# Optimization experiments

Measured on AMD Instinct MI355X. Metric: run time of the kernel, lower is better.

## Reference

```python
import jax, jax.numpy as jnp
import numpy as np

N_SENT, N_DOC, G = 100000, 10000, 32

def _seg_mean_right(x, src, dst, n_dst):
    # DGL GraphConv(norm='right'): sum incoming messages / in_degree (clamped to 1)
    m = jax.ops.segment_sum(x[src], dst, num_segments=n_dst)
    deg = jax.ops.segment_sum(jnp.ones_like(dst, dtype=x.dtype), dst, num_segments=n_dst)
    return m / jnp.maximum(deg, 1.0)[:, None]

def _rel_layer(xs, xd, coeff, basis, loop_w, bias,
               src_ss, dst_ss, src_sd, dst_sd, src_ds, dst_ds):
    # WeightBasis: per-relation weight = sum_b coeff[r,b] * basis[b]
    W = jnp.einsum('rb,bio->rio', coeff, basis)  # [3, in, out]
    # rel 0: sent->doc, rel 1: doc->sent, rel 2: sent->sent; HeteroGraphConv sums per dst ntype
    h_doc = _seg_mean_right(xs, src_sd, dst_sd, N_DOC) @ W[0]
    h_sent = (_seg_mean_right(xd, src_ds, dst_ds, N_SENT) @ W[1]
              + _seg_mean_right(xs, src_ss, dst_ss, N_SENT) @ W[2])
    h_sent = jax.nn.relu(h_sent + xs @ loop_w + bias)
    h_doc = jax.nn.relu(h_doc + xd @ loop_w + bias)
    return h_sent, h_doc

def setup_inputs() -> dict:
    key = jax.random.key(0)
    ks = jax.random.split(key, 20)
    d_in, d_h, d_o = 768, 256, 128
    inp = {
        'x_sent': jax.random.normal(ks[0], (N_SENT, d_in), jnp.float32),
        'x_doc': jax.random.normal(ks[1], (N_DOC, d_in), jnp.float32),
        'coeff1': jax.random.normal(ks[2], (3, 2), jnp.float32),
        'basis1': jax.random.normal(ks[3], (2, d_in, d_h), jnp.float32) * 0.02,
        'loop_w1': jax.random.normal(ks[4], (d_in, d_h), jnp.float32) * 0.02,
        'bias1': jnp.zeros((d_h,), jnp.float32),
        'coeff2': jax.random.normal(ks[5], (3, 2), jnp.float32),
        'basis2': jax.random.normal(ks[6], (2, d_h, d_o), jnp.float32) * 0.05,
        'loop_w2': jax.random.normal(ks[7], (d_h, d_o), jnp.float32) * 0.05,
        'bias2': jnp.zeros((d_o,), jnp.float32),
        'w_score': jax.random.normal(ks[8], (d_o, 1), jnp.float32) * 0.05,
        'b_score': jnp.zeros((1,), jnp.float32),
        'src_ss': jax.random.randint(ks[9], (400000,), 0, N_SENT, jnp.int32),
        'dst_ss': jax.random.randint(ks[10], (400000,), 0, N_SENT, jnp.int32),
        'src_sd': jax.random.randint(ks[11], (100000,), 0, N_SENT, jnp.int32),
        'dst_sd': jax.random.randint(ks[12], (100000,), 0, N_DOC, jnp.int32),
        'src_ds': jax.random.randint(ks[13], (100000,), 0, N_DOC, jnp.int32),
        'dst_ds': jax.random.randint(ks[14], (100000,), 0, N_SENT, jnp.int32),
        'gid_sent': jnp.sort(jax.random.randint(ks[15], (N_SENT,), 0, G, jnp.int32)),
        'gid_doc': jnp.sort(jax.random.randint(ks[16], (N_DOC,), 0, G, jnp.int32)),
        'num_graphs': G,
    }
    return inp

def reference(x_sent, x_doc, coeff1, basis1, loop_w1, bias1,
              coeff2, basis2, loop_w2, bias2, w_score, b_score,
              src_ss, dst_ss, src_sd, dst_sd, src_ds, dst_ds,
              gid_sent, gid_doc, num_graphs):
    h_s, h_d = _rel_layer(x_sent, x_doc, coeff1, basis1, loop_w1, bias1,
                          src_ss, dst_ss, src_sd, dst_sd, src_ds, dst_ds)
    h_s, h_d = _rel_layer(h_s, h_d, coeff2, basis2, loop_w2, bias2,
                          src_ss, dst_ss, src_sd, dst_sd, src_ds, dst_ds)
    # dgl.sum_nodes over batched graph, summed across ntypes
    readout = (jax.ops.segment_sum(h_s, gid_sent, num_segments=num_graphs)
               + jax.ops.segment_sum(h_d, gid_doc, num_segments=num_graphs))
    return readout @ w_score + b_score  # [G, 1]
```

## Files before the change

kernel.cpp:

```cpp
#include <hip/hip_runtime.h>

#define CDIV(a,b) (((a)+(b)-1)/(b))

typedef __attribute__((ext_vector_type(8))) short bf16x8;
typedef __attribute__((ext_vector_type(4))) float floatx4;

__device__ __forceinline__ ushort f2bf(float x) {
    unsigned u = __float_as_uint(x);
    return (ushort)((u + 0x7fffu + ((u >> 16) & 1u)) >> 16);
}
__device__ __forceinline__ float bflo(unsigned v) { return __uint_as_float(v << 16); }
__device__ __forceinline__ float bfhi(unsigned v) { return __uint_as_float(v & 0xffff0000u); }

__device__ __forceinline__ void load_lds16(const ushort* g, ushort* l) {
    __builtin_amdgcn_global_load_lds(
        (const __attribute__((address_space(1))) void*)g,
        (__attribute__((address_space(3))) void*)l, 16, 0, 0);
}



__global__ void zero_f4(float4* __restrict__ p, long long n4) {
    long long i = blockIdx.x * 256LL + threadIdx.x;
    if (i < n4) p[i] = make_float4(0.f, 0.f, 0.f, 0.f);
}

__global__ void fill_w5(ushort* __restrict__ BsT, ushort* __restrict__ BdT,
                        const float* __restrict__ basis, const float* __restrict__ loopw,
                        const float* __restrict__ coeff, int K, int N, long long KN) {
    long long i = blockIdx.x * 256LL + threadIdx.x;
    if (i >= KN) return;
    int k = (int)(i % K), n = (int)(i / K);
    int sec = blockIdx.y;
    float val;
    if (sec == 2 || sec == 4) {
        val = loopw[(size_t)k * N + n];
    } else {
        int r = (sec == 0) ? 0 : (sec == 1) ? 2 : 1;
        val = coeff[2 * r] * basis[(size_t)k * N + n] + coeff[2 * r + 1] * basis[KN + (size_t)k * N + n];
    }
    ushort* dst = (sec < 3) ? BsT : BdT;
    int col0 = (sec == 0) ? 0 : (sec == 1) ? N : (sec == 2) ? 2 * N : (sec == 3) ? 0 : N;
    int nn = col0 + n;
    dst[(size_t)nn * K + (k & ~63) + ((k & 63) ^ ((nn & 7) << 3))] = f2bf(val);
}


__global__ void accum_deg_all(const int* __restrict__ dss, const int* __restrict__ dds,
                              const int* __restrict__ dsd, int nss, int nds, int nsd,
                              int NS, int* __restrict__ deg) {
    int i = blockIdx.x * 256 + threadIdx.x;
    if (i < nss) atomicAdd(&deg[dss[i]], 1);
    else if (i < nss + nds) atomicAdd(&deg[NS + dds[i - nss]], 1);
    else if (i < nss + nds + nsd) atomicAdd(&deg[2 * NS + dsd[i - nss - nds]], 1);
}

__global__ void scan_p1(const int* __restrict__ deg, int n, int* __restrict__ bsum) {
    __shared__ int sd[256];
    int blk = blockIdx.x, tid = threadIdx.x;
    int i0 = blk * 1024 + tid * 4;
    int s = 0;
#pragma unroll
    for (int j = 0; j < 4; ++j) if (i0 + j < n) s += deg[i0 + j];
    sd[tid] = s; __syncthreads();
    for (int o = 128; o; o >>= 1) {
        if (tid < o) sd[tid] += sd[tid + o];
        __syncthreads();
    }
    if (tid == 0) bsum[blk] = sd[0];
}

__global__ void scan_p2(int* __restrict__ bsum, int nb, int* __restrict__ rowptr, int ntot, int etot) {
    __shared__ int sd[256];
    int tid = threadIdx.x;
    int v = (tid < nb) ? bsum[tid] : 0;
    sd[tid] = v; __syncthreads();
    for (int o = 1; o < 256; o <<= 1) {
        int t = (tid >= o) ? sd[tid - o] : 0;
        __syncthreads();
        sd[tid] += t;
        __syncthreads();
    }
    if (tid < nb) bsum[tid] = sd[tid] - v;
    if (tid == 0) rowptr[ntot] = etot;
}

__global__ void scan_p3(const int* __restrict__ deg, int n, const int* __restrict__ bsum,
                        int* __restrict__ rowptr) {
    __shared__ int sd[256];
    int blk = blockIdx.x, tid = threadIdx.x;
    int i0 = blk * 1024 + tid * 4;
    int v[4]; int s = 0;
#pragma unroll
    for (int j = 0; j < 4; ++j) { v[j] = (i0 + j < n) ? deg[i0 + j] : 0; s += v[j]; }
    sd[tid] = s; __syncthreads();
    for (int o = 1; o < 256; o <<= 1) {
        int t = (tid >= o) ? sd[tid - o] : 0;
        __syncthreads();
        sd[tid] += t;
        __syncthreads();
    }
    int excl = bsum[blk] + sd[tid] - s;
#pragma unroll
    for (int j = 0; j < 4; ++j) {
        if (i0 + j < n) rowptr[i0 + j] = excl;
        excl += v[j];
    }
}

__global__ void fill_csr_all(const int* __restrict__ sss, const int* __restrict__ dss,
                             const int* __restrict__ sds, const int* __restrict__ dds,
                             const int* __restrict__ ssd, const int* __restrict__ dsd,
                             int nss, int nds, int nsd, int NS,
                             const int* __restrict__ rowptr, int* __restrict__ fill,
                             int* __restrict__ col) {
    int i = blockIdx.x * 256 + threadIdx.x;
    int d, s;
    if (i < nss) { d = dss[i]; s = sss[i]; }
    else if (i < nss + nds) { int j = i - nss; d = NS + dds[j]; s = sds[j]; }
    else if (i < nss + nds + nsd) { int j = i - nss - nds; d = 2 * NS + dsd[j]; s = ssd[j]; }
    else return;
    int p = rowptr[d] + atomicAdd(&fill[d], 1);
    col[p] = s;
}

template<bool AF32>
__global__ __launch_bounds__(256) void gemm_any(
    const void* __restrict__ Araw, const ushort* __restrict__ Bt, ushort* __restrict__ C,
    int M, int K, int N, int BNX) {
    const int nwg = gridDim.x;
    const int orig = blockIdx.x;
    const int q = nwg >> 3, r = nwg & 7;
    const int xcd = orig & 7, idx = orig >> 3;
    const int wg = (xcd < r ? xcd * (q + 1) : r * (q + 1) + (xcd - r) * q) + idx;
    const int bn = (wg % BNX) * 128;
    const long long bm = (long long)(wg / BNX) * 128LL;

    __shared__ ushort As[128 * 64];
    __shared__ ushort Bs[128 * 64];
    const int tid = threadIdx.x;
    const int lane = tid & 63, wave = tid >> 6;
    const int mo = (wave & 1) * 64, no = (wave >> 1) * 64;
    const int l15 = lane & 15, quad = lane >> 4;
    const int srow = wave * 8 + (lane >> 3);
    const int bch = (lane & 7) * 8;
    floatx4 acc[4][4] = {};

    for (int k0 = 0; k0 < K; k0 += 64) {
#pragma unroll
        for (int t = 0; t < 4; ++t) {
            int row = t * 32 + srow;
            load_lds16(Bt + (size_t)(bn + row) * K + k0 + bch,
                       Bs + (t * 32 + wave * 8) * 64);
        }
        if (AF32) {
            float4 pre[4][2];
#pragma unroll
            for (int j = 0; j < 4; ++j) {
                int s = j * 256 + tid;
                int arow = s >> 3, ach = s & 7;
                long long ar = bm + arow; if (ar >= M) ar = M - 1;
                const float* ap = (const float*)Araw + ar * (size_t)K + k0 + ach * 8;
                pre[j][0] = *(const float4*)ap;
                pre[j][1] = *(const float4*)(ap + 4);
            }
#pragma unroll
            for (int j = 0; j < 4; ++j) {
                int s = j * 256 + tid;
                int arow = s >> 3, ach = s & 7;
                uint4 o;
                o.x = (unsigned)f2bf(pre[j][0].x) | ((unsigned)f2bf(pre[j][0].y) << 16);
                o.y = (unsigned)f2bf(pre[j][0].z) | ((unsigned)f2bf(pre[j][0].w) << 16);
                o.z = (unsigned)f2bf(pre[j][1].x) | ((unsigned)f2bf(pre[j][1].y) << 16);
                o.w = (unsigned)f2bf(pre[j][1].z) | ((unsigned)f2bf(pre[j][1].w) << 16);
                *(uint4*)(As + arow * 64 + ((ach * 8) ^ ((arow & 7) << 3))) = o;
            }
        } else {
#pragma unroll
            for (int t = 0; t < 4; ++t) {
                int row = t * 32 + srow;
                long long ar = bm + row; if (ar >= M) ar = M - 1;
                load_lds16((const ushort*)Araw + ar * (size_t)K + k0 + bch,
                           As + (t * 32 + wave * 8) * 64);
            }
        }
        __syncthreads();
        bf16x8 af[2][4], bfr[2][4];
#pragma unroll
        for (int h = 0; h < 2; ++h) {
#pragma unroll
            for (int mt = 0; mt < 4; ++mt) {
                int row = mo + mt * 16 + l15;
                af[h][mt] = *(const bf16x8*)(As + row * 64 + ((h * 32 + quad * 8) ^ ((row & 7) << 3)));
            }
#pragma unroll
            for (int nt = 0; nt < 4; ++nt) {
                int row = no + nt * 16 + l15;
                bfr[h][nt] = *(const bf16x8*)(Bs + row * 64 + ((h * 32 + quad * 8) ^ ((row & 7) << 3)));
            }
        }
#pragma unroll
        for (int h = 0; h < 2; ++h)
#pragma unroll
            for (int mt = 0; mt < 4; ++mt)
#pragma unroll
                for (int nt = 0; nt < 4; ++nt)
                    acc[mt][nt] = __builtin_amdgcn_mfma_f32_16x16x32_bf16(af[h][mt], bfr[h][nt], acc[mt][nt], 0, 0, 0);
        __syncthreads();
    }
#pragma unroll
    for (int mt = 0; mt < 4; ++mt)
#pragma unroll
        for (int i = 0; i < 4; ++i) {
            long long row = bm + mo + mt * 16 + quad * 4 + i;
            if (row < M) {
#pragma unroll
                for (int nt = 0; nt < 4; ++nt)
                    C[row * (size_t)N + bn + no + nt * 16 + l15] = f2bf(acc[mt][nt][i]);
            }
        }
}


__global__ __launch_bounds__(256) void gather_l1(
    const ushort* __restrict__ ys, const ushort* __restrict__ yd,
    const int* __restrict__ rowptr, const int* __restrict__ col,
    const float* __restrict__ bias, ushort* __restrict__ h1s, ushort* __restrict__ h1d,
    int NS, int ND) {
    int d = blockIdx.x * 4 + (threadIdx.x >> 6);
    int lane = threadIdx.x & 63;
    int cb = lane * 4;
    float b0 = bias[cb], b1 = bias[cb + 1], b2 = bias[cb + 2], b3 = bias[cb + 3];
    if (d < NS) {
        float a0 = 0, a1 = 0, a2 = 0, a3 = 0;
        int s0 = rowptr[d], s1 = rowptr[d + 1];
        int e = s0;
        for (; e + 4 <= s1; e += 4) {
            int sA = col[e], sB = col[e + 1], sC = col[e + 2], sD = col[e + 3];
            uint2 vA = *(const uint2*)(ys + (size_t)sA * 768 + 256 + cb);
            uint2 vB = *(const uint2*)(ys + (size_t)sB * 768 + 256 + cb);
            uint2 vC = *(const uint2*)(ys + (size_t)sC * 768 + 256 + cb);
            uint2 vD = *(const uint2*)(ys + (size_t)sD * 768 + 256 + cb);
            a0 += bflo(vA.x) + bflo(vB.x) + bflo(vC.x) + bflo(vD.x);
            a1 += bfhi(vA.x) + bfhi(vB.x) + bfhi(vC.x) + bfhi(vD.x);
            a2 += bflo(vA.y) + bflo(vB.y) + bflo(vC.y) + bflo(vD.y);
            a3 += bfhi(vA.y) + bfhi(vB.y) + bfhi(vC.y) + bfhi(vD.y);
        }
        for (; e < s1; ++e) {
            int s = col[e];
            uint2 v = *(const uint2*)(ys + (size_t)s * 768 + 256 + cb);
            a0 += bflo(v.x); a1 += bfhi(v.x); a2 += bflo(v.y); a3 += bfhi(v.y);
        }
        float inv = 1.f / (float)max(s1 - s0, 1);
        float m0 = a0 * inv, m1 = a1 * inv, m2 = a2 * inv, m3 = a3 * inv;
        a0 = a1 = a2 = a3 = 0.f;
        int t0 = rowptr[NS + d], t1 = rowptr[NS + d + 1];
        for (e = t0; e < t1; ++e) {
            int s = col[e];
            uint2 v = *(const uint2*)(yd + (size_t)s * 512 + cb);
            a0 += bflo(v.x); a1 += bfhi(v.x); a2 += bflo(v.y); a3 += bfhi(v.y);
        }
        inv = 1.f / (float)max(t1 - t0, 1);
        uint2 lv = *(const uint2*)(ys + (size_t)d * 768 + 512 + cb);
        float h0 = fmaxf(m0 + a0 * inv + bflo(lv.x) + b0, 0.f);
        float h1 = fmaxf(m1 + a1 * inv + bfhi(lv.x) + b1, 0.f);
        float h2 = fmaxf(m2 + a2 * inv + bflo(lv.y) + b2, 0.f);
        float h3 = fmaxf(m3 + a3 * inv + bfhi(lv.y) + b3, 0.f);
        uint2 o;
        o.x = (unsigned)f2bf(h0) | ((unsigned)f2bf(h1) << 16);
        o.y = (unsigned)f2bf(h2) | ((unsigned)f2bf(h3) << 16);
        int pos = (cb & ~63) + ((cb & 63) ^ ((d & 7) << 3));
        *(uint2*)(h1s + (size_t)d * 256 + pos) = o;
    } else if (d < NS + ND) {
        int dd = d - NS;
        float a0 = 0, a1 = 0, a2 = 0, a3 = 0;
        int s0 = rowptr[2 * NS + dd], s1 = rowptr[2 * NS + dd + 1];
        int e = s0;
        for (; e + 4 <= s1; e += 4) {
            int sA = col[e], sB = col[e + 1], sC = col[e + 2], sD = col[e + 3];
            uint2 vA = *(const uint2*)(ys + (size_t)sA * 768 + cb);
            uint2 vB = *(const uint2*)(ys + (size_t)sB * 768 + cb);
            uint2 vC = *(const uint2*)(ys + (size_t)sC * 768 + cb);
            uint2 vD = *(const uint2*)(ys + (size_t)sD * 768 + cb);
            a0 += bflo(vA.x) + bflo(vB.x) + bflo(vC.x) + bflo(vD.x);
            a1 += bfhi(vA.x) + bfhi(vB.x) + bfhi(vC.x) + bfhi(vD.x);
            a2 += bflo(vA.y) + bflo(vB.y) + bflo(vC.y) + bflo(vD.y);
            a3 += bfhi(vA.y) + bfhi(vB.y) + bfhi(vC.y) + bfhi(vD.y);
        }
        for (; e < s1; ++e) {
            int s = col[e];
            uint2 v = *(const uint2*)(ys + (size_t)s * 768 + cb);
            a0 += bflo(v.x); a1 += bfhi(v.x); a2 += bflo(v.y); a3 += bfhi(v.y);
        }
        float inv = 1.f / (float)max(s1 - s0, 1);
        uint2 lv = *(const uint2*)(yd + (size_t)dd * 512 + 256 + cb);
        float h0 = fmaxf(a0 * inv + bflo(lv.x) + b0, 0.f);
        float h1 = fmaxf(a1 * inv + bfhi(lv.x) + b1, 0.f);
        float h2 = fmaxf(a2 * inv + bflo(lv.y) + b2, 0.f);
        float h3 = fmaxf(a3 * inv + bfhi(lv.y) + b3, 0.f);
        uint2 o;
        o.x = (unsigned)f2bf(h0) | ((unsigned)f2bf(h1) << 16);
        o.y = (unsigned)f2bf(h2) | ((unsigned)f2bf(h3) << 16);
        int pos = (cb & ~63) + ((cb & 63) ^ ((dd & 7) << 3));
        *(uint2*)(h1d + (size_t)dd * 256 + pos) = o;
    }
}

__global__ __launch_bounds__(256) void gather_l2(
    const ushort* __restrict__ ys, const ushort* __restrict__ yd,
    const int* __restrict__ rowptr, const int* __restrict__ col,
    const float* __restrict__ bias, const float* __restrict__ w,
    const int* __restrict__ gid_s, const int* __restrict__ gid_d,
    float* __restrict__ out, int NS, int ND, int G) {
    __shared__ float part[4][32];
    const int tid = threadIdx.x;
    const int lane = tid & 63, wv = tid >> 6;
    const int cb = lane * 2;
    const float w0 = w[cb], w1 = w[cb + 1];
    const float b0 = bias[cb], b1 = bias[cb + 1];
    float racc = 0.f;
    const int nw = gridDim.x * 4;
    for (int d = blockIdx.x * 4 + wv; d < NS + ND; d += nw) {
        float h0, h1; int g;
        if (d < NS) {
            float a0 = 0.f, a1 = 0.f;
            int s0 = rowptr[d], s1 = rowptr[d + 1];
            int e = s0;
            for (; e + 4 <= s1; e += 4) {
                int sA = col[e], sB = col[e + 1], sC = col[e + 2], sD = col[e + 3];
                unsigned vA = *(const unsigned*)(ys + (size_t)sA * 384 + 128 + cb);
                unsigned vB = *(const unsigned*)(ys + (size_t)sB * 384 + 128 + cb);
                unsigned vC = *(const unsigned*)(ys + (size_t)sC * 384 + 128 + cb);
                unsigned vD = *(const unsigned*)(ys + (size_t)sD * 384 + 128 + cb);
                a0 += bflo(vA) + bflo(vB) + bflo(vC) + bflo(vD);
                a1 += bfhi(vA) + bfhi(vB) + bfhi(vC) + bfhi(vD);
            }
            for (; e < s1; ++e) {
                int s = col[e];
                unsigned v = *(const unsigned*)(ys + (size_t)s * 384 + 128 + cb);
                a0 += bflo(v); a1 += bfhi(v);
            }
            float inv = 1.f / (float)max(s1 - s0, 1);
            float m0 = a0 * inv, m1 = a1 * inv;
            a0 = 0.f; a1 = 0.f;
            int t0 = rowptr[NS + d], t1 = rowptr[NS + d + 1];
            for (e = t0; e < t1; ++e) {
                int s = col[e];
                unsigned v = *(const unsigned*)(yd + (size_t)s * 256 + cb);
                a0 += bflo(v); a1 += bfhi(v);
            }
            inv = 1.f / (float)max(t1 - t0, 1);
            unsigned lv = *(const unsigned*)(ys + (size_t)d * 384 + 256 + cb);
            h0 = fmaxf(m0 + a0 * inv + bflo(lv) + b0, 0.f);
            h1 = fmaxf(m1 + a1 * inv + bfhi(lv) + b1, 0.f);
            g = gid_s[d];
        } else {
            int dd = d - NS;
            float a0 = 0.f, a1 = 0.f;
            int s0 = rowptr[2 * NS + dd], s1 = rowptr[2 * NS + dd + 1];
            int e = s0;
            for (; e + 4 <= s1; e += 4) {
                int sA = col[e], sB = col[e + 1], sC = col[e + 2], sD = col[e + 3];
                unsigned vA = *(const unsigned*)(ys + (size_t)sA * 384 + cb);
                unsigned vB = *(const unsigned*)(ys + (size_t)sB * 384 + cb);
                unsigned vC = *(const unsigned*)(ys + (size_t)sC * 384 + cb);
                unsigned vD = *(const unsigned*)(ys + (size_t)sD * 384 + cb);
                a0 += bflo(vA) + bflo(vB) + bflo(vC) + bflo(vD);
                a1 += bfhi(vA) + bfhi(vB) + bfhi(vC) + bfhi(vD);
            }
            for (; e < s1; ++e) {
                int s = col[e];
                unsigned v = *(const unsigned*)(ys + (size_t)s * 384 + cb);
                a0 += bflo(v); a1 += bfhi(v);
            }
            float inv = 1.f / (float)max(s1 - s0, 1);
            unsigned lv = *(const unsigned*)(yd + (size_t)dd * 256 + 128 + cb);
            h0 = fmaxf(a0 * inv + bflo(lv) + b0, 0.f);
            h1 = fmaxf(a1 * inv + bfhi(lv) + b1, 0.f);
            g = gid_d[dd];
        }
        float sc = h0 * w0 + h1 * w1;
#pragma unroll
        for (int o = 32; o; o >>= 1) sc += __shfl_down(sc, o);
        sc = __shfl(sc, 0);
        if (lane == g) racc += sc;
    }
    if (lane < 32) part[wv][lane] = racc;
    __syncthreads();
    if (tid < G) atomicAdd(&out[tid], part[0][tid] + part[1][tid] + part[2][tid] + part[3][tid]);
}

__global__ void init_out(float* __restrict__ out, const float* __restrict__ b, int G) {
    int i = threadIdx.x;
    if (i < G) out[i] = b[0];
}


extern "C" void kernel_launch(void* const* d_in, const int* in_sizes, int n_in,
                              void* d_out, int out_size, void* d_ws, size_t ws_size,
                              hipStream_t stream) {
    const float* x_sent = (const float*)d_in[0];
    const float* x_doc  = (const float*)d_in[1];
    const float* coeff1 = (const float*)d_in[2];
    const float* basis1 = (const float*)d_in[3];
    const float* loopw1 = (const float*)d_in[4];
    const float* bias1  = (const float*)d_in[5];
    const float* coeff2 = (const float*)d_in[6];
    const float* basis2 = (const float*)d_in[7];
    const float* loopw2 = (const float*)d_in[8];
    const float* bias2  = (const float*)d_in[9];
    const float* wscore = (const float*)d_in[10];
    const float* bscore = (const float*)d_in[11];
    const int* src_ss = (const int*)d_in[12];
    const int* dst_ss = (const int*)d_in[13];
    const int* src_sd = (const int*)d_in[14];
    const int* dst_sd = (const int*)d_in[15];
    const int* src_ds = (const int*)d_in[16];
    const int* dst_ds = (const int*)d_in[17];
    const int* gid_sent = (const int*)d_in[18];
    const int* gid_doc  = (const int*)d_in[19];

    const int DIN = 768, DH = 256, DOo = 128;
    const int NS = in_sizes[0] / DIN;
    const int ND = in_sizes[1] / DIN;
    const int E_SS = in_sizes[12], E_SD = in_sizes[14], E_DS = in_sizes[16];
    const int NTOT = NS + NS + ND;
    const int ETOT = E_SS + E_DS + E_SD;
    const int G = out_size;
    float* out = (float*)d_out;

    char* base = (char*)d_ws;
    size_t off = 0;
    auto alloc = [&](size_t bytes) -> char* {
        char* p = base + off;
        off = (off + bytes + 255) & ~(size_t)255;
        return p;
    };
    ushort* B1sT = (ushort*)alloc((size_t)768 * 768 * 2);
    ushort* B1dT = (ushort*)alloc((size_t)512 * 768 * 2);
    ushort* B2sT = (ushort*)alloc((size_t)384 * 256 * 2);
    ushort* B2dT = (ushort*)alloc((size_t)256 * 256 * 2);
    ushort* ys1 = (ushort*)alloc((size_t)NS * 768 * 2);
    ushort* yd1 = (ushort*)alloc((size_t)ND * 512 * 2);
    ushort* h1s = (ushort*)alloc((size_t)NS * 256 * 2);
    ushort* h1d = (ushort*)alloc((size_t)ND * 256 * 2);
    ushort* ys2 = (ushort*)alloc((size_t)NS * 384 * 2);
    ushort* yd2 = (ushort*)alloc((size_t)ND * 256 * 2);
    int* deg  = (int*)alloc((size_t)2 * NTOT * 4);
    int* fill = deg + NTOT;
    int* rowptr = (int*)alloc((size_t)(NTOT + 1) * 4);
    int* bsum = (int*)alloc(256 * 4);
    int* colall = (int*)alloc((size_t)ETOT * 4);

    long long t1 = (long long)768 * DH, t2 = (long long)256 * DOo;
    fill_w5<<<dim3((unsigned)CDIV(t1, 256), 5), 256, 0, stream>>>(B1sT, B1dT, basis1, loopw1, coeff1, 768, DH, t1);
    fill_w5<<<dim3((unsigned)CDIV(t2, 256), 5), 256, 0, stream>>>(B2sT, B2dT, basis2, loopw2, coeff2, 256, DOo, t2);

    zero_f4<<<(int)CDIV(2 * NTOT / 4, 256), 256, 0, stream>>>((float4*)deg, 2 * NTOT / 4);
    accum_deg_all<<<CDIV(ETOT, 256), 256, 0, stream>>>(dst_ss, dst_ds, dst_sd, E_SS, E_DS, E_SD, NS, deg);
    int nb = CDIV(NTOT, 1024);
    scan_p1<<<nb, 256, 0, stream>>>(deg, NTOT, bsum);
    scan_p2<<<1, 256, 0, stream>>>(bsum, nb, rowptr, NTOT, ETOT);
    scan_p3<<<nb, 256, 0, stream>>>(deg, NTOT, bsum, rowptr);
    fill_csr_all<<<CDIV(ETOT, 256), 256, 0, stream>>>(src_ss, dst_ss, src_ds, dst_ds, src_sd, dst_sd,
                                                      E_SS, E_DS, E_SD, NS, rowptr, fill, colall);

    {
        int mb = CDIV(NS, 128), mb0 = mb / 2;
        int M0 = mb0 * 128;
        gemm_any<true><<<6 * mb0, 256, 0, stream>>>(x_sent, B1sT, ys1, M0, 768, 768, 6);
        gemm_any<true><<<6 * (mb - mb0), 256, 0, stream>>>(
            x_sent + (size_t)M0 * 768, B1sT, ys1 + (size_t)M0 * 768, NS - M0, 768, 768, 6);
    }
    gemm_any<true><<<4 * CDIV(ND, 128), 256, 0, stream>>>(x_doc, B1dT, yd1, ND, 768, 512, 4);

    gather_l1<<<CDIV(NS + ND, 4), 256, 0, stream>>>(ys1, yd1, rowptr, colall, bias1, h1s, h1d, NS, ND);

    gemm_any<false><<<3 * CDIV(NS, 128), 256, 0, stream>>>(h1s, B2sT, ys2, NS, 256, 384, 3);
    gemm_any<false><<<2 * CDIV(ND, 128), 256, 0, stream>>>(h1d, B2dT, yd2, ND, 256, 256, 2);

    init_out<<<1, 64, 0, stream>>>(out, bscore, G);
    gather_l2<<<1100, 256, 0, stream>>>(ys2, yd2, rowptr, colall, bias2, wscore,
                                        gid_sent, gid_doc, out, NS, ND, G);
}
```

Before: 982.0 us.

## Load GEMM A fragments directly from global and double-buffer B in LDS

The GEMM no longer stages the A tile through LDS. Each wave loads its A fragments straight from global memory, converting fp32 to bf16 in registers where needed, while B is double-buffered in LDS so the next tile's loads overlap compute and one barrier per iteration is dropped. The gather_l1 kernel now writes h1 unswizzled, since the layer-2 GEMM reads A rows directly instead of through the swizzled LDS layout. The trade-off is that A loads become strided 16–32 byte per-lane global reads with no LDS reuse across waves, so each A row is fetched by two waves, and loads sit right before the MFMAs, which adds latency exposure.

```diff
diff --git a/kernel.cpp b/kernel.cpp
--- a/kernel.cpp
+++ b/kernel.cpp
@@ -136,8 +136,7 @@
     const int bn = (wg % BNX) * 128;
     const long long bm = (long long)(wg / BNX) * 128LL;
 
-    __shared__ ushort As[128 * 64];
-    __shared__ ushort Bs[128 * 64];
+    __shared__ ushort Bs[2][128 * 64];
     const int tid = threadIdx.x;
     const int lane = tid & 63, wave = tid >> 6;
     const int mo = (wave & 1) * 64, no = (wave >> 1) * 64;
@@ -146,67 +145,60 @@
     const int bch = (lane & 7) * 8;
     floatx4 acc[4][4] = {};
 
-    for (int k0 = 0; k0 < K; k0 += 64) {
+    size_t aoff[4];
+#pragma unroll
+    for (int mt = 0; mt < 4; ++mt) {
+        long long ar = bm + mo + mt * 16 + l15;
+        if (ar >= M) ar = M - 1;
+        aoff[mt] = (size_t)ar * K;
+    }
+
+    auto stageB = [&](int k0, int buf) {
 #pragma unroll
         for (int t = 0; t < 4; ++t) {
             int row = t * 32 + srow;
             load_lds16(Bt + (size_t)(bn + row) * K + k0 + bch,
-                       Bs + (t * 32 + wave * 8) * 64);
-        }
-        if (AF32) {
-            float4 pre[4][2];
-#pragma unroll
-            for (int j = 0; j < 4; ++j) {
-                int s = j * 256 + tid;
-                int arow = s >> 3, ach = s & 7;
-                long long ar = bm + arow; if (ar >= M) ar = M - 1;
-                const float* ap = (const float*)Araw + ar * (size_t)K + k0 + ach * 8;
-                pre[j][0] = *(const float4*)ap;
-                pre[j][1] = *(const float4*)(ap + 4);
-            }
-#pragma unroll
-            for (int j = 0; j < 4; ++j) {
-                int s = j * 256 + tid;
-                int arow = s >> 3, ach = s & 7;
-                uint4 o;
-                o.x = (unsigned)f2bf(pre[j][0].x) | ((unsigned)f2bf(pre[j][0].y) << 16);
-                o.y = (unsigned)f2bf(pre[j][0].z) | ((unsigned)f2bf(pre[j][0].w) << 16);
-                o.z = (unsigned)f2bf(pre[j][1].x) | ((unsigned)f2bf(pre[j][1].y) << 16);
-                o.w = (unsigned)f2bf(pre[j][1].z) | ((unsigned)f2bf(pre[j][1].w) << 16);
-                *(uint4*)(As + arow * 64 + ((ach * 8) ^ ((arow & 7) << 3))) = o;
-            }
-        } else {
-#pragma unroll
-            for (int t = 0; t < 4; ++t) {
-                int row = t * 32 + srow;
-                long long ar = bm + row; if (ar >= M) ar = M - 1;
-                load_lds16((const ushort*)Araw + ar * (size_t)K + k0 + bch,
-                           As + (t * 32 + wave * 8) * 64);
-            }
-        }
-        __syncthreads();
-        bf16x8 af[2][4], bfr[2][4];
-#pragma unroll
-        for (int h = 0; h < 2; ++h) {
-#pragma unroll
-            for (int mt = 0; mt < 4; ++mt) {
-                int row = mo + mt * 16 + l15;
-                af[h][mt] = *(const bf16x8*)(As + row * 64 + ((h * 32 + quad * 8) ^ ((row & 7) << 3)));
-            }
+                       Bs[buf] + (t * 32 + wave * 8) * 64);
+        }
+    };
+
+    stageB(0, 0);
+    int cur = 0;
+    for (int k0 = 0; k0 < K; k0 += 64) {
+        __syncthreads();
+        if (k0 + 64 < K) stageB(k0 + 64, cur ^ 1);
+        bf16x8 bfr[2][4];
+#pragma unroll
+        for (int h = 0; h < 2; ++h)
 #pragma unroll
             for (int nt = 0; nt < 4; ++nt) {
                 int row = no + nt * 16 + l15;
-                bfr[h][nt] = *(const bf16x8*)(Bs + row * 64 + ((h * 32 + quad * 8) ^ ((row & 7) << 3)));
-            }
-        }
-#pragma unroll
-        for (int h = 0; h < 2; ++h)
-#pragma unroll
-            for (int mt = 0; mt < 4; ++mt)
+                bfr[h][nt] = *(const bf16x8*)(Bs[cur] + row * 64 + ((h * 32 + quad * 8) ^ ((row & 7) << 3)));
+            }
+#pragma unroll
+        for (int h = 0; h < 2; ++h) {
+#pragma unroll
+            for (int mt = 0; mt < 4; ++mt) {
+                bf16x8 af;
+                if (AF32) {
+                    const float* ap = (const float*)Araw + aoff[mt] + k0 + h * 32 + quad * 8;
+                    float4 p0 = *(const float4*)ap;
+                    float4 p1 = *(const float4*)(ap + 4);
+                    unsigned w0 = (unsigned)f2bf(p0.x) | ((unsigned)f2bf(p0.y) << 16);
+                    unsigned w1 = (unsigned)f2bf(p0.z) | ((unsigned)f2bf(p0.w) << 16);
+                    unsigned w2 = (unsigned)f2bf(p1.x) | ((unsigned)f2bf(p1.y) << 16);
+                    unsigned w3 = (unsigned)f2bf(p1.z) | ((unsigned)f2bf(p1.w) << 16);
+                    uint4 packed = make_uint4(w0, w1, w2, w3);
+                    af = *(const bf16x8*)&packed;
+                } else {
+                    af = *(const bf16x8*)((const ushort*)Araw + aoff[mt] + k0 + h * 32 + quad * 8);
+                }
 #pragma unroll
                 for (int nt = 0; nt < 4; ++nt)
-                    acc[mt][nt] = __builtin_amdgcn_mfma_f32_16x16x32_bf16(af[h][mt], bfr[h][nt], acc[mt][nt], 0, 0, 0);
-        __syncthreads();
+                    acc[mt][nt] = __builtin_amdgcn_mfma_f32_16x16x32_bf16(af, bfr[h][nt], acc[mt][nt], 0, 0, 0);
+            }
+        }
+        cur ^= 1;
     }
 #pragma unroll
     for (int mt = 0; mt < 4; ++mt)
@@ -269,8 +261,7 @@
         uint2 o;
         o.x = (unsigned)f2bf(h0) | ((unsigned)f2bf(h1) << 16);
         o.y = (unsigned)f2bf(h2) | ((unsigned)f2bf(h3) << 16);
-        int pos = (cb & ~63) + ((cb & 63) ^ ((d & 7) << 3));
-        *(uint2*)(h1s + (size_t)d * 256 + pos) = o;
+        *(uint2*)(h1s + (size_t)d * 256 + cb) = o;
     } else if (d < NS + ND) {
         int dd = d - NS;
         float a0 = 0, a1 = 0, a2 = 0, a3 = 0;
@@ -301,8 +292,7 @@
         uint2 o;
         o.x = (unsigned)f2bf(h0) | ((unsigned)f2bf(h1) << 16);
         o.y = (unsigned)f2bf(h2) | ((unsigned)f2bf(h3) << 16);
-        int pos = (cb & ~63) + ((cb & 63) ^ ((dd & 7) << 3));
-        *(uint2*)(h1d + (size_t)dd * 256 + pos) = o;
+        *(uint2*)(h1d + (size_t)dd * 256 + cb) = o;
     }
 }
 
```

New measurement: 1.293 ms. +31.7%, slower.
